# Kernel optimization log

Measured on AMD Instinct MI355X. Metric: run time of the kernel, lower is better.

Reference implementation:

```python
import jax, jax.numpy as jnp
import numpy as np

D = 128  # hard-coded hidden dim in MLP_T

def setup_inputs() -> dict:
    key = jax.random.key(0)
    ks = jax.random.split(key, 8)
    N, IN = 16384, 768
    return {
        "x": jax.random.normal(ks[0], (N, IN), dtype=jnp.float32),
        "decay_value": 1,
        "W_token": jax.random.normal(ks[1], (IN, D), dtype=jnp.float32) * (IN ** -0.5),
        "b_token": jax.random.normal(ks[2], (D,), dtype=jnp.float32) * 0.02,
        "W_qkv": jax.random.normal(ks[3], (D, 3 * D), dtype=jnp.float32) * (D ** -0.5),
        "b_qkv": jax.random.normal(ks[4], (3 * D,), dtype=jnp.float32) * 0.02,
        "W_fc": jax.random.normal(ks[5], (D, 1), dtype=jnp.float32) * (D ** -0.5),
        "b_fc": jax.random.normal(ks[6], (1,), dtype=jnp.float32) * 0.02,
    }

def reference(x, decay_value, W_token, b_token, W_qkv, b_qkv, W_fc, b_fc):
    # token projection: [N, in_chan] -> [N, 128]
    h = x @ W_token + b_token
    # qkv: [N, 384] split along feature dim into q, k, v of [N, 128]
    qkv = h @ W_qkv + b_qkv
    q, k, v = qkv[:, :D], qkv[:, D:2 * D], qkv[:, 2 * D:]
    # sigmoid attention (no row normalization); dropout is identity in eval mode
    att_scores = jax.nn.sigmoid(q @ k.T)            # [N, N]
    att = att_scores @ v                            # [N, 128]
    out = att @ W_fc + b_fc                         # [N, 1]
    # GradientReversal is identity in the forward pass
    return out
```

## Files before the change

### kernel.cpp

```cpp
#include <hip/hip_runtime.h>
#include <hip/hip_bf16.h>
#include <stdint.h>

#define N_ROWS 16384

typedef __bf16 bf16x8 __attribute__((ext_vector_type(8)));
typedef float f32x4 __attribute__((ext_vector_type(4)));

#define AS1 __attribute__((address_space(1)))
#define AS3 __attribute__((address_space(3)))

#define OFF_WCS  0u
#define OFF_BC   589824u
#define OFF_QB   591360u
#define OFF_KB   4785664u
#define OFF_WV   8979968u
#define OFF_PART 9045504u

__global__ void prep(const float* __restrict__ Wt, const float* __restrict__ Wq,
                     const float* __restrict__ bt, const float* __restrict__ bq,
                     __bf16* __restrict__ WcS, float* __restrict__ bc) {
    int u = blockIdx.x * 256 + threadIdx.x;
    if (u < 768 * 96) {
        int k = u / 96, n4 = u % 96;
        float s[4] = {0, 0, 0, 0};
        const float* wtp = Wt + k * 128;
        const float* wqp = Wq + n4 * 4;
#pragma unroll 8
        for (int d = 0; d < 128; d++) {
            float a = wtp[d];
            float4 b = *(const float4*)(wqp + d * 384);
            s[0] += a * b.x; s[1] += a * b.y; s[2] += a * b.z; s[3] += a * b.w;
        }
        int kb_ = k >> 6, c = (k >> 3) & 7, k7 = k & 7;
#pragma unroll
        for (int j = 0; j < 4; j++) {
            int n = n4 * 4 + j;
            WcS[n * 768 + kb_ * 64 + ((c ^ (n & 7)) << 3) + k7] = (__bf16)s[j];
        }
    }
    if (u < 384) {
        float s = bq[u];
        for (int d = 0; d < 128; d++) s += bt[d] * Wq[d * 384 + u];
        bc[u] = s;
    }
}

__launch_bounds__(256)
__global__ void gemm_qkv(const float* __restrict__ x, const __bf16* __restrict__ WcS,
                         const float* __restrict__ bc, const float* __restrict__ W_fc,
                         __bf16* __restrict__ qb, __bf16* __restrict__ kb,
                         float* __restrict__ wv) {
    __shared__ float  Asm[64 * 64];
    __shared__ __bf16 Bsm[128 * 64];
    __shared__ float  wred[64];
    const int tid = threadIdx.x, wave = tid >> 6, lane = tid & 63;
    const int n16 = lane & 15, q = lane >> 4;
    const int mh = wave >> 1, nw = wave & 1;
    const int row0 = blockIdx.x * 64;
    const int sp = blockIdx.y;

    const char* aptr[4];
    const char* bptr[4];
    {
        int p = (lane & 15) >> 1, half = lane & 1;
#pragma unroll
        for (int i = 0; i < 4; i++) {
            int ar = row0 + wave * 16 + i * 4 + (lane >> 4);
            aptr[i] = (const char*)x + (size_t)ar * 3072 + ((p ^ (ar & 7)) * 8 + half * 4) * 4;
            int br = sp * 128 + wave * 32 + i * 8 + (lane >> 3);
            bptr[i] = (const char*)WcS + (size_t)br * 1536 + (lane & 7) * 16;
        }
    }
    f32x4 acc[2][4];
#pragma unroll
    for (int mt = 0; mt < 2; mt++)
#pragma unroll
        for (int t = 0; t < 4; t++) acc[mt][t] = (f32x4){0, 0, 0, 0};

    for (int kbi = 0; kbi < 12; kbi++) {
#pragma unroll
        for (int i = 0; i < 4; i++)
            __builtin_amdgcn_global_load_lds((const AS1 void*)(aptr[i] + kbi * 256),
                (AS3 void*)((char*)Asm + wave * 4096 + i * 1024), 16, 0, 0);
#pragma unroll
        for (int i = 0; i < 4; i++)
            __builtin_amdgcn_global_load_lds((const AS1 void*)(bptr[i] + kbi * 128),
                (AS3 void*)((char*)Bsm + wave * 4096 + i * 1024), 16, 0, 0);
        __syncthreads();
#pragma unroll
        for (int ks = 0; ks < 2; ks++) {
            const int swz = ((ks * 4 + q) ^ (n16 & 7)) << 3;
            bf16x8 af[2];
#pragma unroll
            for (int mt = 0; mt < 2; mt++) {
                const float* ap = Asm + (mh * 32 + mt * 16 + n16) * 64 + swz;
                f32x4 a0 = *(const f32x4*)ap;
                f32x4 a1 = *(const f32x4*)(ap + 4);
                bf16x8 t;
                t[0] = (__bf16)a0[0]; t[1] = (__bf16)a0[1]; t[2] = (__bf16)a0[2]; t[3] = (__bf16)a0[3];
                t[4] = (__bf16)a1[0]; t[5] = (__bf16)a1[1]; t[6] = (__bf16)a1[2]; t[7] = (__bf16)a1[3];
                af[mt] = t;
            }
#pragma unroll
            for (int t = 0; t < 4; t++) {
                bf16x8 bf = *(const bf16x8*)(Bsm + (nw * 64 + t * 16 + n16) * 64 + swz);
                acc[0][t] = __builtin_amdgcn_mfma_f32_16x16x32_bf16(af[0], bf, acc[0][t], 0, 0, 0);
                acc[1][t] = __builtin_amdgcn_mfma_f32_16x16x32_bf16(af[1], bf, acc[1][t], 0, 0, 0);
            }
        }
        __syncthreads();
    }

    const int clb = nw * 64 + n16;
    if (sp == 0) {
#pragma unroll
        for (int t = 0; t < 4; t++) {
            int cl = clb + t * 16;
            float bcv = bc[cl];
#pragma unroll
            for (int mt = 0; mt < 2; mt++)
#pragma unroll
                for (int r = 0; r < 4; r++) {
                    int row = row0 + mh * 32 + mt * 16 + q * 4 + r;
                    qb[row * 128 + cl] = (__bf16)((acc[mt][t][r] + bcv) * -1.44269504088896f);
                }
        }
    } else if (sp == 1) {
#pragma unroll
        for (int t = 0; t < 4; t++) {
            int d = clb + t * 16;
            float bcv = bc[128 + d];
#pragma unroll
            for (int mt = 0; mt < 2; mt++)
#pragma unroll
                for (int r = 0; r < 4; r++) {
                    int row = row0 + mh * 32 + mt * 16 + q * 4 + r;
                    kb[row * 128 + (((d >> 3) ^ (row & 15)) << 3) + (d & 7)] = (__bf16)(acc[mt][t][r] + bcv);
                }
        }
    } else {
        float wacc[2][4] = {{0, 0, 0, 0}, {0, 0, 0, 0}};
#pragma unroll
        for (int t = 0; t < 4; t++) {
            int cl = clb + t * 16;
            float bcv = bc[256 + cl];
            float wf = W_fc[cl];
#pragma unroll
            for (int mt = 0; mt < 2; mt++)
#pragma unroll
                for (int r = 0; r < 4; r++) wacc[mt][r] += (acc[mt][t][r] + bcv) * wf;
        }
        float vred[2][4];
#pragma unroll
        for (int mt = 0; mt < 2; mt++)
#pragma unroll
            for (int r = 0; r < 4; r++) {
                float v = wacc[mt][r];
                v += __shfl_xor(v, 1, 64);
                v += __shfl_xor(v, 2, 64);
                v += __shfl_xor(v, 4, 64);
                v += __shfl_xor(v, 8, 64);
                vred[mt][r] = v;
                if (nw == 0 && n16 == 0) wred[mh * 32 + mt * 16 + q * 4 + r] = v;
            }
        __syncthreads();
        if (nw == 1 && n16 == 0) {
#pragma unroll
            for (int mt = 0; mt < 2; mt++)
#pragma unroll
                for (int r = 0; r < 4; r++) {
                    int lr = mh * 32 + mt * 16 + q * 4 + r;
                    wv[row0 + lr] = wred[lr] + vred[mt][r];
                }
        }
    }
}

__launch_bounds__(128)
__global__ void attn(const __bf16* __restrict__ qb, const __bf16* __restrict__ kb,
                     const float* __restrict__ wv, float* __restrict__ partial) {
    __shared__ __bf16 kbuf[128 * 128];
    __shared__ float wbuf[128];
    const int tid = threadIdx.x;
    const int wave = tid >> 6, lane = tid & 63;
    const int n16 = lane & 15, q = lane >> 4;
    const int row0 = blockIdx.x * 128 + wave * 64;
    const int sp = blockIdx.y;
    bf16x8 qf[4][4];
#pragma unroll
    for (int mt = 0; mt < 4; mt++)
#pragma unroll
        for (int ks = 0; ks < 4; ks++)
            qf[mt][ks] = *(const bf16x8*)(qb + (row0 + mt * 16 + n16) * 128 + ks * 32 + q * 8);
    float acc[4][4] = {{0}, {0}, {0}, {0}};
    for (int jc = 0; jc < 16; jc++) {
        const int jbase = sp * 2048 + jc * 128;
        const char* gsrc = (const char*)kb + (size_t)jbase * 256;
#pragma unroll
        for (int i = 0; i < 16; i++) {
            const int off = wave * 16384 + i * 1024;
            __builtin_amdgcn_global_load_lds(
                (const AS1 void*)(gsrc + off + lane * 16),
                (AS3 void*)((char*)kbuf + off), 16, 0, 0);
        }
        if (tid < 128) wbuf[tid] = wv[jbase + tid];
        __syncthreads();
#pragma unroll
        for (int t = 0; t < 8; t++) {
            f32x4 s[4];
#pragma unroll
            for (int mt = 0; mt < 4; mt++) s[mt] = (f32x4){0, 0, 0, 0};
#pragma unroll
            for (int ks = 0; ks < 4; ks++) {
                const int chunk = (ks * 4 + q) ^ n16;
                bf16x8 bf = *(const bf16x8*)(kbuf + (t * 16 + n16) * 128 + chunk * 8);
#pragma unroll
                for (int mt = 0; mt < 4; mt++)
                    s[mt] = __builtin_amdgcn_mfma_f32_16x16x32_bf16(qf[mt][ks], bf, s[mt], 0, 0, 0);
            }
            const float wval = wbuf[t * 16 + n16];
#pragma unroll
            for (int mt = 0; mt < 4; mt++)
#pragma unroll
                for (int r = 0; r < 4; r++)
                    acc[mt][r] += __builtin_amdgcn_rcpf(1.0f + __builtin_amdgcn_exp2f(s[mt][r])) * wval;
        }
        __syncthreads();
    }
#pragma unroll
    for (int mt = 0; mt < 4; mt++)
#pragma unroll
        for (int r = 0; r < 4; r++) {
            float v = acc[mt][r];
            v += __shfl_xor(v, 1, 64);
            v += __shfl_xor(v, 2, 64);
            v += __shfl_xor(v, 4, 64);
            v += __shfl_xor(v, 8, 64);
            if (n16 == 0) partial[sp * N_ROWS + row0 + mt * 16 + q * 4 + r] = v;
        }
}

__global__ void reduce_out(const float* __restrict__ partial, const float* __restrict__ b_fc,
                           float* __restrict__ out) {
    int i = blockIdx.x * 256 + threadIdx.x;
    float v = b_fc[0];
#pragma unroll
    for (int s = 0; s < 8; s++) v += partial[s * N_ROWS + i];
    out[i] = v;
}

extern "C" void kernel_launch(void* const* d_in, const int* in_sizes, int n_in,
                              void* d_out, int out_size, void* d_ws, size_t ws_size,
                              hipStream_t stream) {
    const float* x       = (const float*)d_in[0];
    const float* W_token = (const float*)d_in[2];
    const float* b_token = (const float*)d_in[3];
    const float* W_qkv   = (const float*)d_in[4];
    const float* b_qkv   = (const float*)d_in[5];
    const float* W_fc    = (const float*)d_in[6];
    const float* b_fc    = (const float*)d_in[7];
    float* out = (float*)d_out;
    char* ws = (char*)d_ws;

    __bf16* WcS = (__bf16*)(ws + OFF_WCS);
    float*  bc  = (float*)(ws + OFF_BC);
    __bf16* qb  = (__bf16*)(ws + OFF_QB);
    __bf16* kb  = (__bf16*)(ws + OFF_KB);
    float*  wv  = (float*)(ws + OFF_WV);
    float*  part = (float*)(ws + OFF_PART);

    prep<<<288, 256, 0, stream>>>(W_token, W_qkv, b_token, b_qkv, WcS, bc);
    gemm_qkv<<<dim3(256, 3), 256, 0, stream>>>(x, WcS, bc, W_fc, qb, kb, wv);
    attn<<<dim3(128, 8), 128, 0, stream>>>(qb, kb, wv, part);
    reduce_out<<<64, 256, 0, stream>>>(part, b_fc, out);
}
```

Before: 213.1 us.

## Stream K fragments from global in attention, drop LDS staging and reduce kernel

The attention kernel no longer stages K tiles through shared memory with block barriers. Each wave now loads its K fragments straight from global/L2 into registers, prefetching the next 16-key step while the current one is computed. The K layout loses its XOR swizzle to match these direct loads. The grid is split 16 ways over keys with 256-thread blocks, and partial sums go to the output through atomicAdd. The output is seeded with b_fc inside gemm_qkv, which removes the reduce_out kernel and the partial buffer. The trade-off is extra global/L2 traffic from redundant K reads across waves, plus atomic contention and ordering that is no longer deterministic.

```diff
diff --git a/kernel.cpp b/kernel.cpp
--- a/kernel.cpp
+++ b/kernel.cpp
@@ -15,7 +15,6 @@
 #define OFF_QB   591360u
 #define OFF_KB   4785664u
 #define OFF_WV   8979968u
-#define OFF_PART 9045504u
 
 __global__ void prep(const float* __restrict__ Wt, const float* __restrict__ Wq,
                      const float* __restrict__ bt, const float* __restrict__ bq,
@@ -49,9 +48,10 @@
 __launch_bounds__(256)
 __global__ void gemm_qkv(const float* __restrict__ x, const __bf16* __restrict__ WcS,
                          const float* __restrict__ bc, const float* __restrict__ W_fc,
+                         const float* __restrict__ b_fc,
                          __bf16* __restrict__ qb, __bf16* __restrict__ kb,
-                         float* __restrict__ wv) {
-    __shared__ float  Asm[64 * 64];
+                         float* __restrict__ wv, float* __restrict__ out) {
+    __shared__ float  Asm_[64 * 64];
     __shared__ __bf16 Bsm[128 * 64];
     __shared__ float  wred[64];
     const int tid = threadIdx.x, wave = tid >> 6, lane = tid & 63;
@@ -60,6 +60,8 @@
     const int row0 = blockIdx.x * 64;
     const int sp = blockIdx.y;
 
+    if (sp == 2 && tid < 64) out[row0 + tid] = b_fc[0];
+
     const char* aptr[4];
     const char* bptr[4];
     {
@@ -82,7 +84,7 @@
 #pragma unroll
         for (int i = 0; i < 4; i++)
             __builtin_amdgcn_global_load_lds((const AS1 void*)(aptr[i] + kbi * 256),
-                (AS3 void*)((char*)Asm + wave * 4096 + i * 1024), 16, 0, 0);
+                (AS3 void*)((char*)Asm_ + wave * 4096 + i * 1024), 16, 0, 0);
 #pragma unroll
         for (int i = 0; i < 4; i++)
             __builtin_amdgcn_global_load_lds((const AS1 void*)(bptr[i] + kbi * 128),
@@ -90,20 +92,23 @@
         __syncthreads();
 #pragma unroll
         for (int ks = 0; ks < 2; ks++) {
-            const int swz = ((ks * 4 + q) ^ (n16 & 7)) << 3;
+            const int P = ks * 4 + q;
             bf16x8 af[2];
 #pragma unroll
             for (int mt = 0; mt < 2; mt++) {
-                const float* ap = Asm + (mh * 32 + mt * 16 + n16) * 64 + swz;
-                f32x4 a0 = *(const f32x4*)ap;
-                f32x4 a1 = *(const f32x4*)(ap + 4);
+                const int r = mh * 32 + mt * 16 + n16;
+                const int sa = r & 7;
+                const float* ap = Asm_ + r * 64 + ((P ^ sa) << 3);
+                f32x4 f0 = *(const f32x4*)ap;
+                f32x4 f1 = *(const f32x4*)(ap + 4);
                 bf16x8 t;
-                t[0] = (__bf16)a0[0]; t[1] = (__bf16)a0[1]; t[2] = (__bf16)a0[2]; t[3] = (__bf16)a0[3];
-                t[4] = (__bf16)a1[0]; t[5] = (__bf16)a1[1]; t[6] = (__bf16)a1[2]; t[7] = (__bf16)a1[3];
+                t[0] = (__bf16)f0[0]; t[1] = (__bf16)f0[1]; t[2] = (__bf16)f0[2]; t[3] = (__bf16)f0[3];
+                t[4] = (__bf16)f1[0]; t[5] = (__bf16)f1[1]; t[6] = (__bf16)f1[2]; t[7] = (__bf16)f1[3];
                 af[mt] = t;
             }
 #pragma unroll
             for (int t = 0; t < 4; t++) {
+                const int swz = (P ^ (n16 & 7)) << 3;
                 bf16x8 bf = *(const bf16x8*)(Bsm + (nw * 64 + t * 16 + n16) * 64 + swz);
                 acc[0][t] = __builtin_amdgcn_mfma_f32_16x16x32_bf16(af[0], bf, acc[0][t], 0, 0, 0);
                 acc[1][t] = __builtin_amdgcn_mfma_f32_16x16x32_bf16(af[1], bf, acc[1][t], 0, 0, 0);
@@ -136,7 +141,7 @@
 #pragma unroll
                 for (int r = 0; r < 4; r++) {
                     int row = row0 + mh * 32 + mt * 16 + q * 4 + r;
-                    kb[row * 128 + (((d >> 3) ^ (row & 15)) << 3) + (d & 7)] = (__bf16)(acc[mt][t][r] + bcv);
+                    kb[row * 128 + d] = (__bf16)(acc[mt][t][r] + bcv);
                 }
         }
     } else {
@@ -177,57 +182,58 @@
     }
 }
 
-__launch_bounds__(128)
+__launch_bounds__(256, 3)
 __global__ void attn(const __bf16* __restrict__ qb, const __bf16* __restrict__ kb,
-                     const float* __restrict__ wv, float* __restrict__ partial) {
-    __shared__ __bf16 kbuf[128 * 128];
-    __shared__ float wbuf[128];
+                     const float* __restrict__ wv, float* __restrict__ out) {
     const int tid = threadIdx.x;
     const int wave = tid >> 6, lane = tid & 63;
     const int n16 = lane & 15, q = lane >> 4;
-    const int row0 = blockIdx.x * 128 + wave * 64;
-    const int sp = blockIdx.y;
+    const int row0 = blockIdx.x * 256 + wave * 64;
+    const int jbase = blockIdx.y * 1024;
+
     bf16x8 qf[4][4];
 #pragma unroll
     for (int mt = 0; mt < 4; mt++)
 #pragma unroll
         for (int ks = 0; ks < 4; ks++)
             qf[mt][ks] = *(const bf16x8*)(qb + (row0 + mt * 16 + n16) * 128 + ks * 32 + q * 8);
+
     float acc[4][4] = {{0}, {0}, {0}, {0}};
-    for (int jc = 0; jc < 16; jc++) {
-        const int jbase = sp * 2048 + jc * 128;
-        const char* gsrc = (const char*)kb + (size_t)jbase * 256;
-#pragma unroll
-        for (int i = 0; i < 16; i++) {
-            const int off = wave * 16384 + i * 1024;
-            __builtin_amdgcn_global_load_lds(
-                (const AS1 void*)(gsrc + off + lane * 16),
-                (AS3 void*)((char*)kbuf + off), 16, 0, 0);
-        }
-        if (tid < 128) wbuf[tid] = wv[jbase + tid];
-        __syncthreads();
-#pragma unroll
-        for (int t = 0; t < 8; t++) {
-            f32x4 s[4];
-#pragma unroll
-            for (int mt = 0; mt < 4; mt++) s[mt] = (f32x4){0, 0, 0, 0};
-#pragma unroll
-            for (int ks = 0; ks < 4; ks++) {
-                const int chunk = (ks * 4 + q) ^ n16;
-                bf16x8 bf = *(const bf16x8*)(kbuf + (t * 16 + n16) * 128 + chunk * 8);
-#pragma unroll
-                for (int mt = 0; mt < 4; mt++)
-                    s[mt] = __builtin_amdgcn_mfma_f32_16x16x32_bf16(qf[mt][ks], bf, s[mt], 0, 0, 0);
-            }
-            const float wval = wbuf[t * 16 + n16];
+    const __bf16* kp = kb + (size_t)(jbase + n16) * 128 + q * 8;
+    const float* wp = wv + jbase + n16;
+
+    bf16x8 bcur[4];
+    float wcur;
+#pragma unroll
+    for (int ks = 0; ks < 4; ks++) bcur[ks] = *(const bf16x8*)(kp + ks * 32);
+    wcur = wp[0];
+
+#pragma unroll 2
+    for (int st = 0; st < 64; st++) {
+        bf16x8 bnxt[4];
+        const __bf16* kpn = kp + (size_t)(st + 1) * 2048;
+#pragma unroll
+        for (int ks = 0; ks < 4; ks++) bnxt[ks] = *(const bf16x8*)(kpn + ks * 32);
+        float wnxt = wp[(st + 1) * 16];
+
+        f32x4 sc[4];
+#pragma unroll
+        for (int mt = 0; mt < 4; mt++) sc[mt] = (f32x4){0, 0, 0, 0};
+#pragma unroll
+        for (int ks = 0; ks < 4; ks++)
 #pragma unroll
             for (int mt = 0; mt < 4; mt++)
-#pragma unroll
-                for (int r = 0; r < 4; r++)
-                    acc[mt][r] += __builtin_amdgcn_rcpf(1.0f + __builtin_amdgcn_exp2f(s[mt][r])) * wval;
-        }
-        __syncthreads();
-    }
+                sc[mt] = __builtin_amdgcn_mfma_f32_16x16x32_bf16(qf[mt][ks], bcur[ks], sc[mt], 0, 0, 0);
+#pragma unroll
+        for (int mt = 0; mt < 4; mt++)
+#pragma unroll
+            for (int r = 0; r < 4; r++)
+                acc[mt][r] += __builtin_amdgcn_rcpf(1.0f + __builtin_amdgcn_exp2f(sc[mt][r])) * wcur;
+#pragma unroll
+        for (int ks = 0; ks < 4; ks++) bcur[ks] = bnxt[ks];
+        wcur = wnxt;
+    }
+
 #pragma unroll
     for (int mt = 0; mt < 4; mt++)
 #pragma unroll
@@ -237,17 +243,8 @@
             v += __shfl_xor(v, 2, 64);
             v += __shfl_xor(v, 4, 64);
             v += __shfl_xor(v, 8, 64);
-            if (n16 == 0) partial[sp * N_ROWS + row0 + mt * 16 + q * 4 + r] = v;
-        }
-}
-
-__global__ void reduce_out(const float* __restrict__ partial, const float* __restrict__ b_fc,
-                           float* __restrict__ out) {
-    int i = blockIdx.x * 256 + threadIdx.x;
-    float v = b_fc[0];
-#pragma unroll
-    for (int s = 0; s < 8; s++) v += partial[s * N_ROWS + i];
-    out[i] = v;
+            if (n16 == 0) atomicAdd(&out[row0 + mt * 16 + q * 4 + r], v);
+        }
 }
 
 extern "C" void kernel_launch(void* const* d_in, const int* in_sizes, int n_in,
@@ -268,10 +265,8 @@
     __bf16* qb  = (__bf16*)(ws + OFF_QB);
     __bf16* kb  = (__bf16*)(ws + OFF_KB);
     float*  wv  = (float*)(ws + OFF_WV);
-    float*  part = (float*)(ws + OFF_PART);
 
     prep<<<288, 256, 0, stream>>>(W_token, W_qkv, b_token, b_qkv, WcS, bc);
-    gemm_qkv<<<dim3(256, 3), 256, 0, stream>>>(x, WcS, bc, W_fc, qb, kb, wv);
-    attn<<<dim3(128, 8), 128, 0, stream>>>(qb, kb, wv, part);
-    reduce_out<<<64, 256, 0, stream>>>(part, b_fc, out);
-}
+    gemm_qkv<<<dim3(256, 3), 256, 0, stream>>>(x, WcS, bc, W_fc, b_fc, qb, kb, wv, out);
+    attn<<<dim3(64, 16), 256, 0, stream>>>(qb, kb, wv, out);
+}
```

Result: slower. 248.2 us (+16.4%).
